# Performance work log

Measured on AMD Instinct MI355X. Metric: run time of the kernel, lower is better.

Reference implementation:

```python
import jax, jax.numpy as jnp
import numpy as np

B, T, D_IN, D_OUT = 2, 2048, 2048, 2048
H, KV = 32, 8
HD = D_OUT // H          # 64
G = H // KV              # group_size = 4
ROPE_BASE = 10000.0


def setup_inputs() -> dict:
    key = jax.random.key(0)
    ks = jax.random.split(key, 5)
    s = 0.02  # weight init scale
    return {
        "x":  jax.random.normal(ks[0], (B, T, D_IN), jnp.float32),
        "Wq": jax.random.normal(ks[1], (D_IN, D_OUT), jnp.float32) * s,
        "Wk": jax.random.normal(ks[2], (D_IN, KV * HD), jnp.float32) * s,
        "Wv": jax.random.normal(ks[3], (D_IN, KV * HD), jnp.float32) * s,
        "Wo": jax.random.normal(ks[4], (D_OUT, D_OUT), jnp.float32) * s,
    }


def _rope_cos_sin(t, hd):
    inv = 1.0 / (ROPE_BASE ** (jnp.arange(0, hd, 2, dtype=jnp.float32) / hd))
    ang = jnp.arange(t, dtype=jnp.float32)[:, None] * inv[None, :]  # (T, hd/2)
    return jnp.cos(ang), jnp.sin(ang)


def _apply_rope(x, cos, sin):
    # x: (b, h, T, hd); rotate adjacent pairs (complex multiply, Llama-style)
    xr = x.reshape(x.shape[:-1] + (HD // 2, 2))
    x0, x1 = xr[..., 0], xr[..., 1]
    c = cos[None, None]  # (1,1,T,hd/2)
    s = sin[None, None]
    o0 = x0 * c - x1 * s
    o1 = x0 * s + x1 * c
    return jnp.stack([o0, o1], axis=-1).reshape(x.shape)


def reference(x, Wq, Wk, Wv, Wo):
    b, t, _ = x.shape
    q = (x @ Wq).reshape(b, t, H, HD).transpose(0, 2, 1, 3)    # (b,H,T,hd)
    k = (x @ Wk).reshape(b, t, KV, HD).transpose(0, 2, 1, 3)   # (b,KV,T,hd)
    v = (x @ Wv).reshape(b, t, KV, HD).transpose(0, 2, 1, 3)
    cos, sin = _rope_cos_sin(t, HD)
    q = _apply_rope(q, cos, sin)
    k = _apply_rope(k, cos, sin)
    # GQA: expand KV groups to all heads (repeat_interleave on head dim)
    k = jnp.repeat(k, G, axis=1)  # (b,H,T,hd)
    v = jnp.repeat(v, G, axis=1)
    scores = jnp.einsum('bhqd,bhkd->bhqk', q, k) / jnp.sqrt(jnp.float32(HD))
    causal = jnp.triu(jnp.ones((t, t), dtype=bool), 1)
    scores = jnp.where(causal[None, None], -jnp.inf, scores)
    w = jax.nn.softmax(scores, axis=-1)
    ctx = jnp.einsum('bhqk,bhkd->bqhd', w, v).reshape(b, t, D_OUT)
    return ctx @ Wo
```

## Files before the change

kernel.cpp:

```cpp
#include <hip/hip_runtime.h>

#define TQ 2048
#define NB 2
#define NH 32
#define NKV 8
#define HD 64
#define DIN 2048
#define DOUT 2048
#define NQKV 3072
#define QK_W 2560
#define GK 2048

typedef unsigned short u16;
typedef unsigned int u32;
typedef __attribute__((ext_vector_type(8))) short bf16x8;
typedef __attribute__((ext_vector_type(4))) float f32x4;
typedef __attribute__((ext_vector_type(4))) u16 u16x4;

typedef __attribute__((address_space(1))) const u32 gas_u32;
typedef __attribute__((address_space(3))) u32 las_u32;

#define NEG (-1.0e30f)
#define CL2 0.18033688f

__device__ __forceinline__ u16 f2bf(float f) {
  u32 u = __float_as_uint(f);
  u += 0x7fffu + ((u >> 16) & 1u);
  return (u16)(u >> 16);
}
__device__ __forceinline__ float bf2f(u16 h) { return __uint_as_float(((u32)h) << 16); }
__device__ __forceinline__ u32 cvtpk(float lo, float hi) {
  u32 r;
  asm("v_cvt_pk_bf16_f32 %0, %1, %2" : "=v"(r) : "v"(lo), "v"(hi));
  return r;
}
__device__ __forceinline__ float exp2g(float x) {
  float r;
  asm("v_exp_f32 %0, %1\n\ts_nop 0" : "=v"(r) : "v"(x));
  return r;
}

__device__ __forceinline__ void prep_transpose(const float* __restrict__ src, int nsrc,
                                               u16* __restrict__ dst, int row0, int vb,
                                               float (*tile)[33]) {
  const int nTK = GK / 32;
  int kt = vb % nTK, nt = vb / nTK;
  int k0 = kt * 32, n0 = nt * 32;
  int rr = threadIdx.x >> 5, cc = threadIdx.x & 31;
#pragma unroll
  for (int p = 0; p < 4; ++p) {
    int kl = p * 8 + rr;
    tile[kl][cc] = src[(size_t)(k0 + kl) * nsrc + n0 + cc];
  }
  __syncthreads();
#pragma unroll
  for (int p = 0; p < 4; ++p) {
    int nl = p * 8 + rr;
    dst[(size_t)(row0 + n0 + nl) * GK + k0 + cc] = f2bf(tile[cc][nl]);
  }
}

__global__ __launch_bounds__(256)
void k_prep(const float* __restrict__ x,  const float* __restrict__ Wq,
            const float* __restrict__ Wk, const float* __restrict__ Wv,
            const float* __restrict__ Wo, u16* __restrict__ xb,
            u16* __restrict__ WqkvT, u16* __restrict__ WoT,
            float2* __restrict__ tab) {
  __shared__ float tile[32][33];
  const int bid = blockIdx.x;
  if (bid < 8192) {
    int i = bid * 256 + threadIdx.x;
    f32x4 v = *(const f32x4*)(x + (size_t)i * 4);
    u16x4 o;
    o[0] = f2bf(v[0]); o[1] = f2bf(v[1]); o[2] = f2bf(v[2]); o[3] = f2bf(v[3]);
    *(u16x4*)(xb + (size_t)i * 4) = o;
  } else if (bid < 12288) {
    prep_transpose(Wq, 2048, WqkvT, 0,    bid - 8192,  tile);
  } else if (bid < 13312) {
    prep_transpose(Wk, 512,  WqkvT, 2048, bid - 12288, tile);
  } else if (bid < 14336) {
    prep_transpose(Wv, 512,  WqkvT, 2560, bid - 13312, tile);
  } else if (bid < 18432) {
    prep_transpose(Wo, 2048, WoT,   0,    bid - 14336, tile);
  } else {
    int idx = (bid - 18432) * 256 + threadIdx.x;
    int t = idx >> 5, i = idx & 31;
    float inv = 1.0f / powf(10000.0f, (float)i / 32.0f);
    float ang = (float)t * inv;
    tab[idx] = make_float2(cosf(ang), sinf(ang));
  }
}

template <int MODE>
__global__ __launch_bounds__(256, 2)
void k_gemm(const u16* __restrict__ A, const u16* __restrict__ Bt,
            u16* __restrict__ QKV, u16* __restrict__ Vt, float* __restrict__ Cf,
            const float2* __restrict__ tab, int N) {
  __shared__ __align__(16) u16 lds[2][16384];
  const int tid = threadIdx.x;
  const int lane = tid & 63, wid = tid >> 6;
  const int nTN = N >> 7;
  const int tm = blockIdx.x / nTN, tn = blockIdx.x % nTN;
  const int m0 = tm << 7, n0 = tn << 7;
  const int l15 = lane & 15, lg = lane >> 4;
  const int wr = (wid >> 1) << 6, wc = (wid & 1) << 6;

  f32x4 acc[4][4] = {};

  auto stage = [&](int buf, int k0) {
    u16* base = &lds[buf][0];
#pragma unroll
    for (int p = 0; p < 4; ++p) {
      int c = p * 256 + tid;
      int row = c >> 3, kb = c & 7;
      int ksrc = k0 + ((kb ^ (row & 7)) << 3);
      const u16* sA = A + (size_t)(m0 + row) * GK + ksrc;
      __builtin_amdgcn_global_load_lds((gas_u32*)sA, (las_u32*)(base + c * 8), 16, 0, 0);
      const u16* sB = Bt + (size_t)(n0 + row) * GK + ksrc;
      __builtin_amdgcn_global_load_lds((gas_u32*)sB, (las_u32*)(base + 8192 + c * 8), 16, 0, 0);
    }
  };

  auto compute = [&](int buf) {
    const u16* ldsA = &lds[buf][0];
    const u16* ldsB = &lds[buf][8192];
#pragma unroll
    for (int kk = 0; kk < 2; ++kk) {
      bf16x8 af[4], bfr[4];
#pragma unroll
      for (int m = 0; m < 4; ++m) {
        int row = wr + m * 16 + l15;
        int koff = (kk * 32 + lg * 8) ^ ((row & 7) << 3);
        af[m] = *(const bf16x8*)(ldsA + row * 64 + koff);
      }
#pragma unroll
      for (int n = 0; n < 4; ++n) {
        int row = wc + n * 16 + l15;
        int koff = (kk * 32 + lg * 8) ^ ((row & 7) << 3);
        bfr[n] = *(const bf16x8*)(ldsB + row * 64 + koff);
      }
#pragma unroll
      for (int m = 0; m < 4; ++m)
#pragma unroll
        for (int n = 0; n < 4; ++n)
          acc[m][n] = __builtin_amdgcn_mfma_f32_16x16x32_bf16(af[m], bfr[n], acc[m][n], 0, 0, 0);
    }
  };

  stage(0, 0);
  __syncthreads();
  const int nk = GK / 64;
  for (int t = 0; t < nk; ++t) {
    if (t + 1 < nk) stage((t + 1) & 1, (t + 1) * 64);
    compute(t & 1);
    __syncthreads();
  }

  if (MODE == 1) {
#pragma unroll
    for (int m = 0; m < 4; ++m)
#pragma unroll
      for (int n = 0; n < 4; ++n)
#pragma unroll
        for (int r = 0; r < 4; ++r) {
          int row = m0 + wr + m * 16 + lg * 4 + r;
          int col = n0 + wc + n * 16 + l15;
          Cf[(size_t)row * N + col] = acc[m][n][r];
        }
  } else if (n0 >= 2560) {
#pragma unroll
    for (int m = 0; m < 4; ++m)
#pragma unroll
      for (int n = 0; n < 4; ++n)
#pragma unroll
        for (int r = 0; r < 4; ++r) {
          int row = m0 + wr + m * 16 + lg * 4 + r;
          int col = n0 + wc + n * 16 + l15;
          int dh = col - 2560, kvh = dh >> 6, d = dh & 63;
          int bb = row >> 11, tt = row & 2047;
          Vt[(((size_t)bb * NKV + kvh) * 64 + d) * TQ + tt] = f2bf(acc[m][n][r]);
        }
  } else {
#pragma unroll
    for (int m = 0; m < 4; ++m)
#pragma unroll
      for (int n = 0; n < 4; ++n) {
        int col = n0 + wc + n * 16 + l15;
        int dh = (col & 63) >> 1;
        float sgn = (col & 1) ? 1.0f : -1.0f;
#pragma unroll
        for (int r = 0; r < 4; ++r) {
          int row = m0 + wr + m * 16 + lg * 4 + r;
          float a = acc[m][n][r];
          float b = __shfl_xor(a, 1);
          int t = row & (TQ - 1);
          float2 csv = tab[t * 32 + dh];
          float o = a * csv.x + sgn * b * csv.y;
          QKV[(size_t)row * QK_W + col] = f2bf(o);
        }
      }
  }
}

__global__ __launch_bounds__(256, 3)
void k_attn(const u16* __restrict__ QKV, const u16* __restrict__ Vt, u16* __restrict__ ctx) {
  __shared__ __align__(16) u16 Ksh[2][4096];
  __shared__ __align__(16) u16 Vsh[2][4096];
  __shared__ __align__(16) u16 Psh[4][2048];
  const int tid = threadIdx.x, lane = tid & 63, w = tid >> 6;
  const int l15 = lane & 15, lg = lane >> 4;
  const int bid = blockIdx.x;
  const int qt = 15 - (bid >> 6);
  const int hb = bid & 63;
  const int h = hb & 31, b = hb >> 5;
  const int kvh = h >> 2;
  const int q0 = qt << 7;
  const int qb = q0 + w * 32;
  const size_t rowbase = (size_t)b * TQ;
  const u16* Vg = Vt + ((size_t)(b * NKV + kvh)) * 64 * TQ;

  auto stage = [&](int buf, int kv0) {
    u16* kd = &Ksh[buf][0];
    u16* vd = &Vsh[buf][0];
#pragma unroll
    for (int p = 0; p < 2; ++p) {
      int c = p * 256 + tid;
      int row = c >> 3, kb = c & 7;
      int off = (kb ^ (row & 7)) << 3;
      const u16* sK = QKV + (rowbase + kv0 + row) * QK_W + 2048 + kvh * 64 + off;
      __builtin_amdgcn_global_load_lds((gas_u32*)sK, (las_u32*)(kd + c * 8), 16, 0, 0);
      const u16* sV = Vg + (size_t)row * TQ + kv0 + off;
      __builtin_amdgcn_global_load_lds((gas_u32*)sV, (las_u32*)(vd + c * 8), 16, 0, 0);
    }
  };

  bf16x8 qf[2][2];
#pragma unroll
  for (int m = 0; m < 2; ++m)
#pragma unroll
    for (int kk = 0; kk < 2; ++kk)
      qf[m][kk] = *(const bf16x8*)(QKV + (rowbase + qb + m * 16 + l15) * QK_W + h * 64 + kk * 32 + lg * 8);

  float m_run[2] = {NEG, NEG}, l_run[2] = {0.f, 0.f};
  f32x4 oacc[2][4] = {};

  stage(0, 0);
  const int nt = 2 * qt + 2;
  for (int t = 0; t < nt; ++t) {
    const int kv0 = t << 6;
    __syncthreads();
    if (t + 1 < nt) stage((t + 1) & 1, kv0 + 64);
    if (kv0 > qb + 31) continue;

    const u16* Kl = &Ksh[t & 1][0];
    const u16* Vl = &Vsh[t & 1][0];

    f32x4 stv[2][4];
#pragma unroll
    for (int c = 0; c < 4; ++c) {
      const int krow = c * 16 + l15;
      const int ks = (krow & 7) << 3;
      f32x4 z0 = {}, z1 = {};
#pragma unroll
      for (int kk = 0; kk < 2; ++kk) {
        bf16x8 kf = *(const bf16x8*)(Kl + krow * 64 + ((kk * 32 + lg * 8) ^ ks));
        z0 = __builtin_amdgcn_mfma_f32_16x16x32_bf16(kf, qf[0][kk], z0, 0, 0, 0);
        z1 = __builtin_amdgcn_mfma_f32_16x16x32_bf16(kf, qf[1][kk], z1, 0, 0, 0);
      }
      stv[0][c] = z0; stv[1][c] = z1;
    }

    const bool maskT = (kv0 + 63 > qb);
    float mt[2];
    if (maskT) {
#pragma unroll
      for (int m = 0; m < 2; ++m) {
        const int qpos = qb + m * 16 + l15;
        float mx = NEG;
#pragma unroll
        for (int c = 0; c < 4; ++c)
#pragma unroll
          for (int r = 0; r < 4; ++r) {
            int kvpos = kv0 + c * 16 + lg * 4 + r;
            float sv = stv[m][c][r];
            sv = (kvpos > qpos) ? NEG : sv;
            stv[m][c][r] = sv;
            mx = fmaxf(mx, sv);
          }
        mt[m] = mx;
      }
    } else {
#pragma unroll
      for (int m = 0; m < 2; ++m) {
        float mx = NEG;
#pragma unroll
        for (int c = 0; c < 4; ++c)
#pragma unroll
          for (int r = 0; r < 4; ++r) mx = fmaxf(mx, stv[m][c][r]);
        mt[m] = mx;
      }
    }
#pragma unroll
    for (int m = 0; m < 2; ++m) {
      mt[m] = fmaxf(mt[m], __shfl_xor(mt[m], 16));
      mt[m] = fmaxf(mt[m], __shfl_xor(mt[m], 32));
    }

    if (__any((mt[0] > m_run[0] + 64.0f) || (mt[1] > m_run[1] + 64.0f))) {
#pragma unroll
      for (int m = 0; m < 2; ++m) {
        float nm = fmaxf(m_run[m], mt[m]);
        float sc = exp2g((m_run[m] - nm) * CL2);
        m_run[m] = nm;
        l_run[m] *= sc;
#pragma unroll
        for (int dt = 0; dt < 4; ++dt) oacc[m][dt] *= sc;
      }
    }

    u16* Pw = &Psh[w][0];
#pragma unroll
    for (int m = 0; m < 2; ++m) {
      const float msc = m_run[m] * CL2;
      float ssum = 0.f;
      const int rowp = m * 16 + l15;
      const int swz = (l15 & 7) << 3;
#pragma unroll
      for (int c = 0; c < 4; ++c) {
        float p0 = exp2g(stv[m][c][0] * CL2 - msc);
        float p1 = exp2g(stv[m][c][1] * CL2 - msc);
        float p2 = exp2g(stv[m][c][2] * CL2 - msc);
        float p3 = exp2g(stv[m][c][3] * CL2 - msc);
        ssum += (p0 + p1) + (p2 + p3);
        const int kvb = (c * 16 + lg * 4) ^ swz;
        *(u32*)(Pw + rowp * 64 + kvb)       = cvtpk(p0, p1);
        *(u32*)(Pw + rowp * 64 + (kvb | 2)) = cvtpk(p2, p3);
      }
      ssum += __shfl_xor(ssum, 16);
      ssum += __shfl_xor(ssum, 32);
      l_run[m] += ssum;
    }

    bf16x8 pf[2][2];
#pragma unroll
    for (int m = 0; m < 2; ++m)
#pragma unroll
      for (int kc = 0; kc < 2; ++kc)
        pf[m][kc] = *(const bf16x8*)(Pw + (m * 16 + l15) * 64 + ((kc * 32 + lg * 8) ^ ((l15 & 7) << 3)));
#pragma unroll
    for (int dt = 0; dt < 4; ++dt) {
      const int vrow = dt * 16 + l15;
      const int vs = (vrow & 7) << 3;
#pragma unroll
      for (int kc = 0; kc < 2; ++kc) {
        bf16x8 vf = *(const bf16x8*)(Vl + vrow * 64 + ((kc * 32 + lg * 8) ^ vs));
        oacc[0][dt] = __builtin_amdgcn_mfma_f32_16x16x32_bf16(vf, pf[0][kc], oacc[0][dt], 0, 0, 0);
        oacc[1][dt] = __builtin_amdgcn_mfma_f32_16x16x32_bf16(vf, pf[1][kc], oacc[1][dt], 0, 0, 0);
      }
    }
  }

#pragma unroll
  for (int m = 0; m < 2; ++m) {
    float inv = 1.0f / l_run[m];
    size_t row = rowbase + qb + m * 16 + l15;
#pragma unroll
    for (int dt = 0; dt < 4; ++dt) {
      int col = h * 64 + dt * 16 + lg * 4;
      u32 w0 = cvtpk(oacc[m][dt][0] * inv, oacc[m][dt][1] * inv);
      u32 w1 = cvtpk(oacc[m][dt][2] * inv, oacc[m][dt][3] * inv);
      *(u32*)(ctx + row * DOUT + col) = w0;
      *(u32*)(ctx + row * DOUT + col + 2) = w1;
    }
  }
}

extern "C" void kernel_launch(void* const* d_in, const int* in_sizes, int n_in,
                              void* d_out, int out_size, void* d_ws, size_t ws_size,
                              hipStream_t stream) {
  const float* x  = (const float*)d_in[0];
  const float* Wq = (const float*)d_in[1];
  const float* Wk = (const float*)d_in[2];
  const float* Wv = (const float*)d_in[3];
  const float* Wo = (const float*)d_in[4];
  float* out = (float*)d_out;

  char* ws = (char*)d_ws;
  size_t off = 0;
  auto alloc = [&](size_t bytes) -> void* {
    void* p = ws + off;
    off += (bytes + 255) & ~(size_t)255;
    return p;
  };
  const int rows = NB * TQ;
  u16*    xb    = (u16*)alloc((size_t)rows * DIN * 2);
  u16*    WqkvT = (u16*)alloc((size_t)NQKV * GK * 2);
  u16*    WoT   = (u16*)alloc((size_t)DOUT * GK * 2);
  u16*    QKV   = (u16*)alloc((size_t)rows * QK_W * 2);
  u16*    Vt    = (u16*)alloc((size_t)NB * NKV * 64 * TQ * 2);
  u16*    ctx   = (u16*)alloc((size_t)rows * DOUT * 2);
  float2* tab   = (float2*)alloc((size_t)TQ * 32 * sizeof(float2));

  k_prep<<<dim3(18688), dim3(256), 0, stream>>>(x, Wq, Wk, Wv, Wo, xb, WqkvT, WoT, tab);
  k_gemm<0><<<dim3((rows / 128) * (NQKV / 128)), dim3(256), 0, stream>>>(xb, WqkvT, QKV, Vt, nullptr, tab, NQKV);
  k_attn<<<dim3(NB * NH * (TQ / 128)), dim3(256), 0, stream>>>(QKV, Vt, ctx);
  k_gemm<1><<<dim3((rows / 128) * (DOUT / 128)), dim3(256), 0, stream>>>(ctx, WoT, nullptr, nullptr, out, nullptr, DOUT);
}
```

Measured before the change: 184.9 us.

## Process all four GQA query heads per block to share K/V tiles

Reorganizes the attention kernel so each block handles one KV head and a 64-row query tile covering all four query heads in the group, with each wave doing 16 rows across four heads. K/V tiles staged in LDS are reused by four heads, cutting global K/V traffic fourfold. The grid becomes 512 blocks instead of 1024, which reduces parallelism and removes the per-wave early skip for fully masked tiles. Register use also grows with four accumulators per wave.

Result: slower. 283.6 us (+53.4%).

```diff
diff --git a/kernel.cpp b/kernel.cpp
--- a/kernel.cpp
+++ b/kernel.cpp
@@ -206,16 +206,15 @@
 void k_attn(const u16* __restrict__ QKV, const u16* __restrict__ Vt, u16* __restrict__ ctx) {
   __shared__ __align__(16) u16 Ksh[2][4096];
   __shared__ __align__(16) u16 Vsh[2][4096];
-  __shared__ __align__(16) u16 Psh[4][2048];
+  __shared__ __align__(16) u16 Psh[4][2][1024];
   const int tid = threadIdx.x, lane = tid & 63, w = tid >> 6;
   const int l15 = lane & 15, lg = lane >> 4;
   const int bid = blockIdx.x;
-  const int qt = 15 - (bid >> 6);
-  const int hb = bid & 63;
-  const int h = hb & 31, b = hb >> 5;
-  const int kvh = h >> 2;
-  const int q0 = qt << 7;
-  const int qb = q0 + w * 32;
+  const int qt = 31 - (bid >> 4);
+  const int rem = bid & 15;
+  const int kvh = rem & 7, b = rem >> 3;
+  const int q0 = qt << 6;
+  const int qb = q0 + w * 16;
   const size_t rowbase = (size_t)b * TQ;
   const u16* Vg = Vt + ((size_t)(b * NKV + kvh)) * 64 * TQ;
 
@@ -234,141 +233,123 @@
     }
   };
 
-  bf16x8 qf[2][2];
-#pragma unroll
-  for (int m = 0; m < 2; ++m)
+  bf16x8 qf[4][2];
+#pragma unroll
+  for (int hp = 0; hp < 4; ++hp)
 #pragma unroll
     for (int kk = 0; kk < 2; ++kk)
-      qf[m][kk] = *(const bf16x8*)(QKV + (rowbase + qb + m * 16 + l15) * QK_W + h * 64 + kk * 32 + lg * 8);
-
-  float m_run[2] = {NEG, NEG}, l_run[2] = {0.f, 0.f};
-  f32x4 oacc[2][4] = {};
+      qf[hp][kk] = *(const bf16x8*)(QKV + (rowbase + qb + l15) * QK_W +
+                                    (kvh * 4 + hp) * 64 + kk * 32 + lg * 8);
+
+  float m_run[4] = {NEG, NEG, NEG, NEG}, l_run[4] = {0.f, 0.f, 0.f, 0.f};
+  f32x4 oacc[4][4] = {};
 
   stage(0, 0);
-  const int nt = 2 * qt + 2;
+  const int nt = qt + 1;
   for (int t = 0; t < nt; ++t) {
     const int kv0 = t << 6;
     __syncthreads();
     if (t + 1 < nt) stage((t + 1) & 1, kv0 + 64);
-    if (kv0 > qb + 31) continue;
 
     const u16* Kl = &Ksh[t & 1][0];
     const u16* Vl = &Vsh[t & 1][0];
-
-    f32x4 stv[2][4];
-#pragma unroll
-    for (int c = 0; c < 4; ++c) {
-      const int krow = c * 16 + l15;
-      const int ks = (krow & 7) << 3;
-      f32x4 z0 = {}, z1 = {};
-#pragma unroll
-      for (int kk = 0; kk < 2; ++kk) {
-        bf16x8 kf = *(const bf16x8*)(Kl + krow * 64 + ((kk * 32 + lg * 8) ^ ks));
-        z0 = __builtin_amdgcn_mfma_f32_16x16x32_bf16(kf, qf[0][kk], z0, 0, 0, 0);
-        z1 = __builtin_amdgcn_mfma_f32_16x16x32_bf16(kf, qf[1][kk], z1, 0, 0, 0);
-      }
-      stv[0][c] = z0; stv[1][c] = z1;
-    }
-
     const bool maskT = (kv0 + 63 > qb);
-    float mt[2];
-    if (maskT) {
-#pragma unroll
-      for (int m = 0; m < 2; ++m) {
-        const int qpos = qb + m * 16 + l15;
-        float mx = NEG;
+    const int swz = (l15 & 7) << 3;
+
+#pragma unroll
+    for (int hp = 0; hp < 4; ++hp) {
+      f32x4 stv[4];
+#pragma unroll
+      for (int c = 0; c < 4; ++c) {
+        const int krow = c * 16 + l15;
+        const int ks = (krow & 7) << 3;
+        f32x4 z = {};
+#pragma unroll
+        for (int kk = 0; kk < 2; ++kk) {
+          bf16x8 kf = *(const bf16x8*)(Kl + krow * 64 + ((kk * 32 + lg * 8) ^ ks));
+          z = __builtin_amdgcn_mfma_f32_16x16x32_bf16(kf, qf[hp][kk], z, 0, 0, 0);
+        }
+        stv[c] = z;
+      }
+
+      float mx = NEG;
+      if (maskT) {
+        const int qpos = qb + l15;
 #pragma unroll
         for (int c = 0; c < 4; ++c)
 #pragma unroll
           for (int r = 0; r < 4; ++r) {
             int kvpos = kv0 + c * 16 + lg * 4 + r;
-            float sv = stv[m][c][r];
+            float sv = stv[c][r];
             sv = (kvpos > qpos) ? NEG : sv;
-            stv[m][c][r] = sv;
+            stv[c][r] = sv;
             mx = fmaxf(mx, sv);
           }
-        mt[m] = mx;
-      }
-    } else {
-#pragma unroll
-      for (int m = 0; m < 2; ++m) {
-        float mx = NEG;
+      } else {
 #pragma unroll
         for (int c = 0; c < 4; ++c)
 #pragma unroll
-          for (int r = 0; r < 4; ++r) mx = fmaxf(mx, stv[m][c][r]);
-        mt[m] = mx;
-      }
-    }
-#pragma unroll
-    for (int m = 0; m < 2; ++m) {
-      mt[m] = fmaxf(mt[m], __shfl_xor(mt[m], 16));
-      mt[m] = fmaxf(mt[m], __shfl_xor(mt[m], 32));
-    }
-
-    if (__any((mt[0] > m_run[0] + 64.0f) || (mt[1] > m_run[1] + 64.0f))) {
-#pragma unroll
-      for (int m = 0; m < 2; ++m) {
-        float nm = fmaxf(m_run[m], mt[m]);
-        float sc = exp2g((m_run[m] - nm) * CL2);
-        m_run[m] = nm;
-        l_run[m] *= sc;
-#pragma unroll
-        for (int dt = 0; dt < 4; ++dt) oacc[m][dt] *= sc;
-      }
-    }
-
-    u16* Pw = &Psh[w][0];
-#pragma unroll
-    for (int m = 0; m < 2; ++m) {
-      const float msc = m_run[m] * CL2;
-      float ssum = 0.f;
-      const int rowp = m * 16 + l15;
-      const int swz = (l15 & 7) << 3;
-#pragma unroll
-      for (int c = 0; c < 4; ++c) {
-        float p0 = exp2g(stv[m][c][0] * CL2 - msc);
-        float p1 = exp2g(stv[m][c][1] * CL2 - msc);
-        float p2 = exp2g(stv[m][c][2] * CL2 - msc);
-        float p3 = exp2g(stv[m][c][3] * CL2 - msc);
-        ssum += (p0 + p1) + (p2 + p3);
-        const int kvb = (c * 16 + lg * 4) ^ swz;
-        *(u32*)(Pw + rowp * 64 + kvb)       = cvtpk(p0, p1);
-        *(u32*)(Pw + rowp * 64 + (kvb | 2)) = cvtpk(p2, p3);
-      }
-      ssum += __shfl_xor(ssum, 16);
-      ssum += __shfl_xor(ssum, 32);
-      l_run[m] += ssum;
-    }
-
-    bf16x8 pf[2][2];
-#pragma unroll
-    for (int m = 0; m < 2; ++m)
+          for (int r = 0; r < 4; ++r) mx = fmaxf(mx, stv[c][r]);
+      }
+      mx = fmaxf(mx, __shfl_xor(mx, 16));
+      mx = fmaxf(mx, __shfl_xor(mx, 32));
+
+      if (__any(mx > m_run[hp] + 64.0f)) {
+        float nm = fmaxf(m_run[hp], mx);
+        float sc = exp2g((m_run[hp] - nm) * CL2);
+        m_run[hp] = nm;
+        l_run[hp] *= sc;
+#pragma unroll
+        for (int dt = 0; dt < 4; ++dt) oacc[hp][dt] *= sc;
+      }
+
+      u16* Pw = &Psh[w][hp & 1][0];
+      {
+        const float msc = m_run[hp] * CL2;
+        float ssum = 0.f;
+#pragma unroll
+        for (int c = 0; c < 4; ++c) {
+          float p0 = exp2g(stv[c][0] * CL2 - msc);
+          float p1 = exp2g(stv[c][1] * CL2 - msc);
+          float p2 = exp2g(stv[c][2] * CL2 - msc);
+          float p3 = exp2g(stv[c][3] * CL2 - msc);
+          ssum += (p0 + p1) + (p2 + p3);
+          const int kvb = (c * 16 + lg * 4) ^ swz;
+          *(u32*)(Pw + l15 * 64 + kvb)       = cvtpk(p0, p1);
+          *(u32*)(Pw + l15 * 64 + (kvb | 2)) = cvtpk(p2, p3);
+        }
+        ssum += __shfl_xor(ssum, 16);
+        ssum += __shfl_xor(ssum, 32);
+        l_run[hp] += ssum;
+      }
+
+      bf16x8 pf[2];
 #pragma unroll
       for (int kc = 0; kc < 2; ++kc)
-        pf[m][kc] = *(const bf16x8*)(Pw + (m * 16 + l15) * 64 + ((kc * 32 + lg * 8) ^ ((l15 & 7) << 3)));
+        pf[kc] = *(const bf16x8*)(Pw + l15 * 64 + ((kc * 32 + lg * 8) ^ swz));
+#pragma unroll
+      for (int dt = 0; dt < 4; ++dt) {
+        const int vrow = dt * 16 + l15;
+        const int vs = (vrow & 7) << 3;
+#pragma unroll
+        for (int kc = 0; kc < 2; ++kc) {
+          bf16x8 vf = *(const bf16x8*)(Vl + vrow * 64 + ((kc * 32 + lg * 8) ^ vs));
+          oacc[hp][dt] = __builtin_amdgcn_mfma_f32_16x16x32_bf16(vf, pf[kc], oacc[hp][dt], 0, 0, 0);
+        }
+      }
+    }
+  }
+
+#pragma unroll
+  for (int hp = 0; hp < 4; ++hp) {
+    float inv = 1.0f / l_run[hp];
+    size_t row = rowbase + qb + l15;
+    int hcol = (kvh * 4 + hp) * 64;
 #pragma unroll
     for (int dt = 0; dt < 4; ++dt) {
-      const int vrow = dt * 16 + l15;
-      const int vs = (vrow & 7) << 3;
-#pragma unroll
-      for (int kc = 0; kc < 2; ++kc) {
-        bf16x8 vf = *(const bf16x8*)(Vl + vrow * 64 + ((kc * 32 + lg * 8) ^ vs));
-        oacc[0][dt] = __builtin_amdgcn_mfma_f32_16x16x32_bf16(vf, pf[0][kc], oacc[0][dt], 0, 0, 0);
-        oacc[1][dt] = __builtin_amdgcn_mfma_f32_16x16x32_bf16(vf, pf[1][kc], oacc[1][dt], 0, 0, 0);
-      }
-    }
-  }
-
-#pragma unroll
-  for (int m = 0; m < 2; ++m) {
-    float inv = 1.0f / l_run[m];
-    size_t row = rowbase + qb + m * 16 + l15;
-#pragma unroll
-    for (int dt = 0; dt < 4; ++dt) {
-      int col = h * 64 + dt * 16 + lg * 4;
-      u32 w0 = cvtpk(oacc[m][dt][0] * inv, oacc[m][dt][1] * inv);
-      u32 w1 = cvtpk(oacc[m][dt][2] * inv, oacc[m][dt][3] * inv);
+      int col = hcol + dt * 16 + lg * 4;
+      u32 w0 = cvtpk(oacc[hp][dt][0] * inv, oacc[hp][dt][1] * inv);
+      u32 w1 = cvtpk(oacc[hp][dt][2] * inv, oacc[hp][dt][3] * inv);
       *(u32*)(ctx + row * DOUT + col) = w0;
       *(u32*)(ctx + row * DOUT + col + 2) = w1;
     }
@@ -403,6 +384,6 @@
 
   k_prep<<<dim3(18688), dim3(256), 0, stream>>>(x, Wq, Wk, Wv, Wo, xb, WqkvT, WoT, tab);
   k_gemm<0><<<dim3((rows / 128) * (NQKV / 128)), dim3(256), 0, stream>>>(xb, WqkvT, QKV, Vt, nullptr, tab, NQKV);
-  k_attn<<<dim3(NB * NH * (TQ / 128)), dim3(256), 0, stream>>>(QKV, Vt, ctx);
+  k_attn<<<dim3(NB * NKV * (TQ / 64)), dim3(256), 0, stream>>>(QKV, Vt, ctx);
   k_gemm<1><<<dim3((rows / 128) * (DOUT / 128)), dim3(256), 0, stream>>>(ctx, WoT, nullptr, nullptr, out, nullptr, DOUT);
 }
```
